# Optimization experiments

Measured on AMD Instinct MI355X. Metric: run time of the kernel, lower is better.

## Reference

```python
import jax, jax.numpy as jnp
import numpy as np

B, M, F, E = 64, 1024, 4, 256      # batch, memory length, tokens-per-memory-cell, emb_size
NW, HOPS, PL = 32000, 3, 128       # vocab, hops, profile_len


def _embed(table, idx):
    # nn.Embedding with padding_idx=0 -> index 0 maps to zero vector
    return table[idx] * (idx != 0)[..., None].astype(table.dtype)


def _gru_step(x, h, Wih, Whh, bih, bhh):
    # single-step PyTorch GRU cell
    gi = x @ Wih.T + bih
    gh = h @ Whh.T + bhh
    ir, iz, i_n = jnp.split(gi, 3, axis=-1)
    hr, hz, h_n = jnp.split(gh, 3, axis=-1)
    r = jax.nn.sigmoid(ir + hr)
    z = jax.nn.sigmoid(iz + hz)
    n = jnp.tanh(i_n + r * h_n)
    return (1.0 - z) * n + z * h


def setup_inputs() -> dict:
    key = jax.random.key(0)
    ks = jax.random.split(key, 13)
    # HOPS+1 unique embedding tables: A[0..hops-1] plus C[hops-1]; C[h]=tables[h+1] (weight tying)
    tables = (jax.random.normal(ks[0], (HOPS + 1, NW, E)) * 0.1).at[:, 0, :].set(0.0)
    s = 1.0 / np.sqrt(E)
    Wih = jax.random.uniform(ks[1], (3 * E, E), minval=-s, maxval=s)
    Whh = jax.random.uniform(ks[2], (3 * E, E), minval=-s, maxval=s)
    bih = jax.random.uniform(ks[3], (3 * E,), minval=-s, maxval=s)
    bhh = jax.random.uniform(ks[4], (3 * E,), minval=-s, maxval=s)
    sp = 1.0 / np.sqrt(PL)
    Wp = jax.random.uniform(ks[5], (E, PL), minval=-sp, maxval=sp)
    bp = jax.random.uniform(ks[6], (E,), minval=-sp, maxval=sp)
    sv = 1.0 / np.sqrt(2 * E)
    Wv = jax.random.uniform(ks[7], (NW, 2 * E), minval=-sv, maxval=sv)
    bv = jax.random.uniform(ks[8], (NW,), minval=-sv, maxval=sv)
    context = jax.random.randint(ks[9], (B, M, F), 0, NW)
    y_ = jax.random.randint(ks[10], (B,), 0, NW)
    h_ = jax.random.normal(ks[11], (1, B, E))
    profile_encoding = jax.random.normal(ks[12], (B, PL))
    return dict(tables=tables, Wih=Wih, Whh=Whh, bih=bih, bhh=bhh, Wp=Wp, bp=bp,
                Wv=Wv, bv=bv, context=context, y_=y_, h_=h_,
                profile_encoding=profile_encoding)


def reference(tables, Wih, Whh, bih, bhh, Wp, bp, Wv, bv, context, y_, h_, profile_encoding):
    # load_memory (eval mode: no word dropout): memories[h] = sum over F of table[h] embeddings
    ctx = context.reshape(B, M * F)
    mems = [_embed(tables[hop], ctx).reshape(B, M, F, E).sum(axis=2) for hop in range(HOPS + 1)]
    # decoder step
    m = _embed(tables[1], y_)                    # C[0](y_)
    h = _gru_step(m, h_[0], Wih, Whh, bih, bhh)  # [B, E]
    q = h
    p = p_vocab = p_resto = None
    for hop in range(HOPS):
        p_ = mems[hop] * q[:, None, :]           # [B, M, E] elementwise attention scores
        p = p_.sum(axis=2)                        # [B, M]
        attn = jax.nn.softmax(p, axis=1)
        o = jnp.einsum('bm,bme->be', attn, mems[hop + 1])
        if hop == 0:
            p_vocab = jnp.concatenate([h, o], axis=1) @ Wv.T + bv  # uses q[0]=h
        if hop == 1:
            enc = profile_encoding @ Wp.T + bp   # [B, E]
            p_resto = jnp.einsum('bme,be->bm', p_, enc)
        q = q + o
    return p, p_vocab, p_resto, h[None]          # p_ptr, p_vocab, p_resto, h [1,B,E]
```

## Files before the change

kernel.cpp:

```cpp
#include <hip/hip_runtime.h>
#include <cstdint>

#define B_ 64
#define M_ 1024
#define F_ 4
#define E_ 256
#define NW_ 32000
#define PL_ 128

#define P_OFF   0
#define PV_OFF  65536
#define PR_OFF  2113536
#define H_OFF   2179072

typedef unsigned short u16;
typedef unsigned int u32;

typedef __bf16 bf16x8 __attribute__((ext_vector_type(8)));
typedef float f32x4 __attribute__((ext_vector_type(4)));

__device__ __forceinline__ u16 f2bf(float f) {
    u32 x = __builtin_bit_cast(u32, f);
    u32 r = (x + 0x7fffu + ((x >> 16) & 1u)) >> 16;
    return (u16)r;
}

__device__ __forceinline__ bf16x8 pack_bf8(float4 a, float4 b) {
    union { u16 s[8]; bf16x8 v; } u;
    u.s[0] = f2bf(a.x); u.s[1] = f2bf(a.y); u.s[2] = f2bf(a.z); u.s[3] = f2bf(a.w);
    u.s[4] = f2bf(b.x); u.s[5] = f2bf(b.y); u.s[6] = f2bf(b.z); u.s[7] = f2bf(b.w);
    return u.v;
}

__global__ __launch_bounds__(256) void k_gru(
    const float* __restrict__ tables, const float* __restrict__ Wih,
    const float* __restrict__ Whh, const float* __restrict__ bih,
    const float* __restrict__ bhh, const float* __restrict__ Wp,
    const float* __restrict__ bp, const int* __restrict__ y,
    const float* __restrict__ h_, const float* __restrict__ pe,
    float* __restrict__ q0, float* __restrict__ enc, float* __restrict__ outh)
{
    int b = blockIdx.x, t = threadIdx.x;
    __shared__ float m_s[E_], h_s[E_], pe_s[PL_];
    int yb = y[b];
    m_s[t] = tables[(size_t)NW_ * E_ + (size_t)yb * E_ + t];
    h_s[t] = h_[b * E_ + t];
    if (t < PL_) pe_s[t] = pe[b * PL_ + t];
    __syncthreads();

    float g_i[3], g_h[3];
#pragma unroll
    for (int g = 0; g < 3; g++) {
        int j = g * E_ + t;
        float ai = bih[j];
        float ah = bhh[j];
        const float4* wi = (const float4*)(Wih + (size_t)j * E_);
        const float4* wh = (const float4*)(Whh + (size_t)j * E_);
#pragma unroll 8
        for (int e = 0; e < E_ / 4; e++) {
            float4 a = wi[e], c = wh[e];
            ai += a.x * m_s[4 * e] + a.y * m_s[4 * e + 1] +
                  a.z * m_s[4 * e + 2] + a.w * m_s[4 * e + 3];
            ah += c.x * h_s[4 * e] + c.y * h_s[4 * e + 1] +
                  c.z * h_s[4 * e + 2] + c.w * h_s[4 * e + 3];
        }
        g_i[g] = ai; g_h[g] = ah;
    }
    float r = 1.f / (1.f + expf(-(g_i[0] + g_h[0])));
    float z = 1.f / (1.f + expf(-(g_i[1] + g_h[1])));
    float n = tanhf(g_i[2] + r * g_h[2]);
    float hv = (1.f - z) * n + z * h_s[t];
    q0[b * E_ + t] = hv;
    outh[b * E_ + t] = hv;

    float ea = bp[t];
    const float4* wp = (const float4*)(Wp + (size_t)t * PL_);
#pragma unroll 8
    for (int p = 0; p < PL_ / 4; p++) {
        float4 a = wp[p];
        ea += a.x * pe_s[4 * p] + a.y * pe_s[4 * p + 1] +
              a.z * pe_s[4 * p + 2] + a.w * pe_s[4 * p + 3];
    }
    enc[b * E_ + t] = ea;
}

template <int MODE>
__global__ __launch_bounds__(256) void k_scores(
    const float* __restrict__ tab, const int* __restrict__ ctx,
    const float* __restrict__ q, const float* __restrict__ enc,
    float* __restrict__ p_ws, float* __restrict__ out)
{
    int b = blockIdx.y, grp = blockIdx.x;
    int lane = threadIdx.x & 63, w = threadIdx.x >> 6;
    int e0 = lane * 4;
    const float4 qv = *(const float4*)(q + b * E_ + e0);
    float4 qe = make_float4(0.f, 0.f, 0.f, 0.f);
    if (MODE == 1) {
        const float4 ev = *(const float4*)(enc + b * E_ + e0);
        qe = make_float4(qv.x * ev.x, qv.y * ev.y, qv.z * ev.z, qv.w * ev.w);
    }
    int mbase = grp * 32 + w * 8;
    const int4* cp = (const int4*)(ctx + ((size_t)b * M_ + mbase) * 4);
    int4 c[8];
#pragma unroll
    for (int i = 0; i < 8; i++) c[i] = cp[i];

    float pa[8], pr[8];
#pragma unroll
    for (int i = 0; i < 8; i++) {
        const float4 t0 = *(const float4*)(tab + (size_t)c[i].x * E_ + e0);
        const float4 t1 = *(const float4*)(tab + (size_t)c[i].y * E_ + e0);
        const float4 t2 = *(const float4*)(tab + (size_t)c[i].z * E_ + e0);
        const float4 t3 = *(const float4*)(tab + (size_t)c[i].w * E_ + e0);
        float rx = t0.x + t1.x + t2.x + t3.x;
        float ry = t0.y + t1.y + t2.y + t3.y;
        float rz = t0.z + t1.z + t2.z + t3.z;
        float rw = t0.w + t1.w + t2.w + t3.w;
        pa[i] = rx * qv.x + ry * qv.y + rz * qv.z + rw * qv.w;
        if (MODE == 1) pr[i] = rx * qe.x + ry * qe.y + rz * qe.z + rw * qe.w;
    }
#pragma unroll
    for (int o = 32; o > 0; o >>= 1) {
#pragma unroll
        for (int i = 0; i < 8; i++) {
            pa[i] += __shfl_xor(pa[i], o, 64);
            if (MODE == 1) pr[i] += __shfl_xor(pr[i], o, 64);
        }
    }
    if (lane == 0) {
#pragma unroll
        for (int i = 0; i < 8; i++) {
            if (MODE == 2) out[P_OFF + (size_t)b * M_ + mbase + i] = pa[i];
            else           p_ws[(size_t)b * M_ + mbase + i] = pa[i];
            if (MODE == 1) out[PR_OFF + (size_t)b * M_ + mbase + i] = pr[i];
        }
    }
}

__global__ __launch_bounds__(256) void k_soft(
    float* __restrict__ p_ws, const float* __restrict__ qcur,
    float* __restrict__ qnext)
{
    int b = blockIdx.x, t = threadIdx.x;
    __shared__ float red[256];
    float4 v = *(const float4*)(p_ws + (size_t)b * M_ + t * 4);
    float lm = fmaxf(fmaxf(v.x, v.y), fmaxf(v.z, v.w));
    red[t] = lm;
    __syncthreads();
    for (int s = 128; s > 0; s >>= 1) {
        if (t < s) red[t] = fmaxf(red[t], red[t + s]);
        __syncthreads();
    }
    float mx = red[0];
    __syncthreads();
    float e0 = expf(v.x - mx), e1 = expf(v.y - mx);
    float e2 = expf(v.z - mx), e3 = expf(v.w - mx);
    red[t] = e0 + e1 + e2 + e3;
    __syncthreads();
    for (int s = 128; s > 0; s >>= 1) {
        if (t < s) red[t] += red[t + s];
        __syncthreads();
    }
    float inv = 1.f / red[0];
    float4 o = make_float4(e0 * inv, e1 * inv, e2 * inv, e3 * inv);
    *(float4*)(p_ws + (size_t)b * M_ + t * 4) = o;
    qnext[b * E_ + t] = qcur[b * E_ + t];
}

__global__ __launch_bounds__(256) void k_opart(
    const float* __restrict__ tabC, const int* __restrict__ ctx,
    const float* __restrict__ attn, float* __restrict__ qnext)
{
    int b = blockIdx.y, ch = blockIdx.x;
    int lane = threadIdx.x & 63, w = threadIdx.x >> 6;
    int e0 = lane * 4;
    int mbase = ch * 32 + w * 8;

    const int4* cp = (const int4*)(ctx + ((size_t)b * M_ + mbase) * 4);
    int4 c[8];
#pragma unroll
    for (int i = 0; i < 8; i++) c[i] = cp[i];
    const float4* ap = (const float4*)(attn + (size_t)b * M_ + mbase);
    float4 a01 = ap[0], a23 = ap[1];
    float wg[8] = {a01.x, a01.y, a01.z, a01.w, a23.x, a23.y, a23.z, a23.w};

    float4 acc0 = make_float4(0.f, 0.f, 0.f, 0.f);
    float4 acc1 = make_float4(0.f, 0.f, 0.f, 0.f);
#pragma unroll
    for (int i = 0; i < 8; i += 2) {
        const float4 t0 = *(const float4*)(tabC + (size_t)c[i].x * E_ + e0);
        const float4 t1 = *(const float4*)(tabC + (size_t)c[i].y * E_ + e0);
        const float4 t2 = *(const float4*)(tabC + (size_t)c[i].z * E_ + e0);
        const float4 t3 = *(const float4*)(tabC + (size_t)c[i].w * E_ + e0);
        const float4 u0 = *(const float4*)(tabC + (size_t)c[i + 1].x * E_ + e0);
        const float4 u1 = *(const float4*)(tabC + (size_t)c[i + 1].y * E_ + e0);
        const float4 u2 = *(const float4*)(tabC + (size_t)c[i + 1].z * E_ + e0);
        const float4 u3 = *(const float4*)(tabC + (size_t)c[i + 1].w * E_ + e0);
        float w0 = wg[i], w1 = wg[i + 1];
        acc0.x += w0 * (t0.x + t1.x + t2.x + t3.x);
        acc0.y += w0 * (t0.y + t1.y + t2.y + t3.y);
        acc0.z += w0 * (t0.z + t1.z + t2.z + t3.z);
        acc0.w += w0 * (t0.w + t1.w + t2.w + t3.w);
        acc1.x += w1 * (u0.x + u1.x + u2.x + u3.x);
        acc1.y += w1 * (u0.y + u1.y + u2.y + u3.y);
        acc1.z += w1 * (u0.z + u1.z + u2.z + u3.z);
        acc1.w += w1 * (u0.w + u1.w + u2.w + u3.w);
    }
    float4 acc = make_float4(acc0.x + acc1.x, acc0.y + acc1.y,
                             acc0.z + acc1.z, acc0.w + acc1.w);
    __shared__ float red[4][E_];
    *(float4*)&red[w][e0] = acc;
    __syncthreads();
    int t = threadIdx.x;
    float s = red[0][t] + red[1][t] + red[2][t] + red[3][t];
    atomicAdd(qnext + b * E_ + t, s);
}

__global__ __launch_bounds__(256) void k_pvocab(
    const float* __restrict__ Wv, const float* __restrict__ bv,
    const float* __restrict__ q0, const float* __restrict__ q1,
    float* __restrict__ out)
{
    __shared__ u16 X[64 * 512];
    int t = threadIdx.x;
#pragma unroll
    for (int it = 0; it < 16; it++) {
        int id = t + it * 256;
        int bb = id >> 6, c = id & 63;
        float v[8];
        if (c < 32) {
            const float* s = q0 + bb * E_ + c * 8;
#pragma unroll
            for (int j = 0; j < 8; j++) v[j] = s[j];
        } else {
            const float* s1 = q1 + bb * E_ + (c - 32) * 8;
            const float* s0 = q0 + bb * E_ + (c - 32) * 8;
#pragma unroll
            for (int j = 0; j < 8; j++) v[j] = s1[j] - s0[j];
        }
        u32 ww[4];
#pragma unroll
        for (int j = 0; j < 4; j++)
            ww[j] = (u32)f2bf(v[2 * j]) | ((u32)f2bf(v[2 * j + 1]) << 16);
        uint4 uv = make_uint4(ww[0], ww[1], ww[2], ww[3]);
        *(uint4*)(&X[bb * 512 + ((c ^ (bb & 7)) << 3)]) = uv;
    }
    __syncthreads();

    int lane = t & 63, w = t >> 6;
    int n0 = blockIdx.x * 128 + w * 32;
    int l15 = lane & 15, quad = lane >> 4;
    f32x4 acc[4][2];
#pragma unroll
    for (int mt = 0; mt < 4; mt++)
#pragma unroll
        for (int nt = 0; nt < 2; nt++)
            acc[mt][nt] = f32x4{0.f, 0.f, 0.f, 0.f};

    for (int ks = 0; ks < 16; ks++) {
        bf16x8 a[4], bfr[2];
#pragma unroll
        for (int mt = 0; mt < 4; mt++) {
            int m = mt * 16 + l15;
            int c = ks * 4 + quad;
            a[mt] = *(const bf16x8*)(&X[m * 512 + ((c ^ (m & 7)) << 3)]);
        }
#pragma unroll
        for (int nt = 0; nt < 2; nt++) {
            int n = n0 + nt * 16 + l15;
            const float4* wp = (const float4*)(Wv + (size_t)n * 512 + ks * 32 + quad * 8);
            bfr[nt] = pack_bf8(wp[0], wp[1]);
        }
#pragma unroll
        for (int mt = 0; mt < 4; mt++)
#pragma unroll
            for (int nt = 0; nt < 2; nt++)
                acc[mt][nt] = __builtin_amdgcn_mfma_f32_16x16x32_bf16(
                    a[mt], bfr[nt], acc[mt][nt], 0, 0, 0);
    }
#pragma unroll
    for (int nt = 0; nt < 2; nt++) {
        int n = n0 + nt * 16 + l15;
        float bvv = bv[n];
#pragma unroll
        for (int mt = 0; mt < 4; mt++) {
#pragma unroll
            for (int j = 0; j < 4; j++) {
                int m = mt * 16 + quad * 4 + j;
                out[PV_OFF + (size_t)m * 32000 + n] = acc[mt][nt][j] + bvv;
            }
        }
    }
}

extern "C" void kernel_launch(void* const* d_in, const int* in_sizes, int n_in,
                              void* d_out, int out_size, void* d_ws, size_t ws_size,
                              hipStream_t stream)
{
    const float* tables = (const float*)d_in[0];
    const float* Wih = (const float*)d_in[1];
    const float* Whh = (const float*)d_in[2];
    const float* bih = (const float*)d_in[3];
    const float* bhh = (const float*)d_in[4];
    const float* Wp  = (const float*)d_in[5];
    const float* bp  = (const float*)d_in[6];
    const float* Wv  = (const float*)d_in[7];
    const float* bv  = (const float*)d_in[8];
    const int* ctx = (const int*)d_in[9];
    const int* y   = (const int*)d_in[10];
    const float* h_  = (const float*)d_in[11];
    const float* pe  = (const float*)d_in[12];
    float* out = (float*)d_out;

    float* Wf   = (float*)d_ws;
    float* q    = Wf;
    float* enc  = Wf + 65536;
    float* p_ws = Wf + 81920;

    const size_t TSZ = (size_t)NW_ * E_;

    k_gru<<<64, 256, 0, stream>>>(tables, Wih, Whh, bih, bhh, Wp, bp, y, h_, pe,
                                  q, enc, out + H_OFF);
    k_scores<0><<<dim3(32, 64), 256, 0, stream>>>(tables, ctx, q, enc, p_ws, out);
    k_soft<<<64, 256, 0, stream>>>(p_ws, q, q + 16384);
    k_opart<<<dim3(32, 64), 256, 0, stream>>>(tables + TSZ, ctx, p_ws, q + 16384);
    k_scores<1><<<dim3(32, 64), 256, 0, stream>>>(tables + TSZ, ctx, q + 16384,
                                                  enc, p_ws, out);
    k_soft<<<64, 256, 0, stream>>>(p_ws, q + 16384, q + 32768);
    k_opart<<<dim3(32, 64), 256, 0, stream>>>(tables + 2 * TSZ, ctx, p_ws, q + 32768);
    k_scores<2><<<dim3(32, 64), 256, 0, stream>>>(tables + 2 * TSZ, ctx, q + 32768,
                                                  enc, p_ws, out);
    k_pvocab<<<250, 256, 0, stream>>>(Wv, bv, q, q + 16384, out);
}
```

Measured before the change: 458.4 us.

## Convert embedding tables to bf16 and materialize mems1/mems2 once for reuse

Adds a per-call conversion kernel that casts the three used embedding tables to bf16, interleaving tables 1 and 2 per row. A new kernel gathers tables 1 and 2 together, writes the summed memory cells to bf16 buffers mems1/mems2, and computes the hop-0 output. Later hops read these materialized memories with contiguous loads instead of re-gathering four embedding rows per cell. This is meant to cut gather traffic, but it costs a full-table conversion pass every call and gives up precision to bf16 for the memories and the table-0 scores.

```diff
diff --git a/kernel.cpp b/kernel.cpp
--- a/kernel.cpp
+++ b/kernel.cpp
@@ -24,12 +24,51 @@
     u32 r = (x + 0x7fffu + ((x >> 16) & 1u)) >> 16;
     return (u16)r;
 }
-
+__device__ __forceinline__ float bflo(u32 v) {
+    return __builtin_bit_cast(float, v << 16);
+}
+__device__ __forceinline__ float bfhi(u32 v) {
+    return __builtin_bit_cast(float, v & 0xffff0000u);
+}
+__device__ __forceinline__ float dot8(uint4 u, float4 qa, float4 qb) {
+    return bflo(u.x) * qa.x + bfhi(u.x) * qa.y + bflo(u.y) * qa.z + bfhi(u.y) * qa.w +
+           bflo(u.z) * qb.x + bfhi(u.z) * qb.y + bflo(u.w) * qb.z + bfhi(u.w) * qb.w;
+}
+__device__ __forceinline__ void acc8(uint4 u, float* a) {
+    a[0] += bflo(u.x); a[1] += bfhi(u.x); a[2] += bflo(u.y); a[3] += bfhi(u.y);
+    a[4] += bflo(u.z); a[5] += bfhi(u.z); a[6] += bflo(u.w); a[7] += bfhi(u.w);
+}
+__device__ __forceinline__ uint4 pack8(const float* s) {
+    uint4 u;
+    u.x = (u32)f2bf(s[0]) | ((u32)f2bf(s[1]) << 16);
+    u.y = (u32)f2bf(s[2]) | ((u32)f2bf(s[3]) << 16);
+    u.z = (u32)f2bf(s[4]) | ((u32)f2bf(s[5]) << 16);
+    u.w = (u32)f2bf(s[6]) | ((u32)f2bf(s[7]) << 16);
+    return u;
+}
 __device__ __forceinline__ bf16x8 pack_bf8(float4 a, float4 b) {
     union { u16 s[8]; bf16x8 v; } u;
     u.s[0] = f2bf(a.x); u.s[1] = f2bf(a.y); u.s[2] = f2bf(a.z); u.s[3] = f2bf(a.w);
     u.s[4] = f2bf(b.x); u.s[5] = f2bf(b.y); u.s[6] = f2bf(b.z); u.s[7] = f2bf(b.w);
     return u.v;
+}
+
+__global__ __launch_bounds__(256) void k_conv(
+    const float* __restrict__ tables, u16* __restrict__ t0b, u16* __restrict__ t12)
+{
+    int t = blockIdx.y;
+    int c = blockIdx.x * 256 + threadIdx.x;
+    const float* src = tables + (size_t)t * NW_ * E_ + (size_t)c * 8;
+    float4 a = *(const float4*)src;
+    float4 b = *(const float4*)(src + 4);
+    float s[8] = {a.x, a.y, a.z, a.w, b.x, b.y, b.z, b.w};
+    uint4 u = pack8(s);
+    if (t == 0) {
+        *(uint4*)(t0b + (size_t)c * 8) = u;
+    } else {
+        int row = c >> 5, e = (c & 31) * 8;
+        *(uint4*)(t12 + (size_t)row * 512 + (t - 1) * 256 + e) = u;
+    }
 }
 
 __global__ __launch_bounds__(256) void k_gru(
@@ -52,8 +91,7 @@
 #pragma unroll
     for (int g = 0; g < 3; g++) {
         int j = g * E_ + t;
-        float ai = bih[j];
-        float ah = bhh[j];
+        float ai = bih[j], ah = bhh[j];
         const float4* wi = (const float4*)(Wih + (size_t)j * E_);
         const float4* wh = (const float4*)(Whh + (size_t)j * E_);
 #pragma unroll 8
@@ -84,57 +122,37 @@
     enc[b * E_ + t] = ea;
 }
 
-template <int MODE>
-__global__ __launch_bounds__(256) void k_scores(
-    const float* __restrict__ tab, const int* __restrict__ ctx,
-    const float* __restrict__ q, const float* __restrict__ enc,
-    float* __restrict__ p_ws, float* __restrict__ out)
+__global__ __launch_bounds__(256) void k_scores0(
+    const u16* __restrict__ t0b, const int* __restrict__ ctx,
+    const float* __restrict__ q, float* __restrict__ p_ws)
 {
     int b = blockIdx.y, grp = blockIdx.x;
     int lane = threadIdx.x & 63, w = threadIdx.x >> 6;
-    int e0 = lane * 4;
-    const float4 qv = *(const float4*)(q + b * E_ + e0);
-    float4 qe = make_float4(0.f, 0.f, 0.f, 0.f);
-    if (MODE == 1) {
-        const float4 ev = *(const float4*)(enc + b * E_ + e0);
-        qe = make_float4(qv.x * ev.x, qv.y * ev.y, qv.z * ev.z, qv.w * ev.w);
-    }
+    int h = lane >> 5, l32 = lane & 31, e0 = l32 * 8;
+    float4 qa = *(const float4*)(q + b * E_ + e0);
+    float4 qb = *(const float4*)(q + b * E_ + e0 + 4);
     int mbase = grp * 32 + w * 8;
     const int4* cp = (const int4*)(ctx + ((size_t)b * M_ + mbase) * 4);
     int4 c[8];
 #pragma unroll
     for (int i = 0; i < 8; i++) c[i] = cp[i];
 
-    float pa[8], pr[8];
+    float pa[8];
 #pragma unroll
     for (int i = 0; i < 8; i++) {
-        const float4 t0 = *(const float4*)(tab + (size_t)c[i].x * E_ + e0);
-        const float4 t1 = *(const float4*)(tab + (size_t)c[i].y * E_ + e0);
-        const float4 t2 = *(const float4*)(tab + (size_t)c[i].z * E_ + e0);
-        const float4 t3 = *(const float4*)(tab + (size_t)c[i].w * E_ + e0);
-        float rx = t0.x + t1.x + t2.x + t3.x;
-        float ry = t0.y + t1.y + t2.y + t3.y;
-        float rz = t0.z + t1.z + t2.z + t3.z;
-        float rw = t0.w + t1.w + t2.w + t3.w;
-        pa[i] = rx * qv.x + ry * qv.y + rz * qv.z + rw * qv.w;
-        if (MODE == 1) pr[i] = rx * qe.x + ry * qe.y + rz * qe.z + rw * qe.w;
-    }
-#pragma unroll
-    for (int o = 32; o > 0; o >>= 1) {
-#pragma unroll
-        for (int i = 0; i < 8; i++) {
-            pa[i] += __shfl_xor(pa[i], o, 64);
-            if (MODE == 1) pr[i] += __shfl_xor(pr[i], o, 64);
-        }
-    }
-    if (lane == 0) {
-#pragma unroll
-        for (int i = 0; i < 8; i++) {
-            if (MODE == 2) out[P_OFF + (size_t)b * M_ + mbase + i] = pa[i];
-            else           p_ws[(size_t)b * M_ + mbase + i] = pa[i];
-            if (MODE == 1) out[PR_OFF + (size_t)b * M_ + mbase + i] = pr[i];
-        }
-    }
+        int ia = h ? c[i].y : c[i].x;
+        int ib = h ? c[i].w : c[i].z;
+        uint4 ra = *(const uint4*)(t0b + (size_t)ia * E_ + e0);
+        uint4 rb = *(const uint4*)(t0b + (size_t)ib * E_ + e0);
+        pa[i] = dot8(ra, qa, qb) + dot8(rb, qa, qb);
+    }
+#pragma unroll
+    for (int o = 32; o > 0; o >>= 1)
+#pragma unroll
+        for (int i = 0; i < 8; i++) pa[i] += __shfl_xor(pa[i], o, 64);
+    if (lane == 0)
+#pragma unroll
+        for (int i = 0; i < 8; i++) p_ws[(size_t)b * M_ + mbase + i] = pa[i];
 }
 
 __global__ __launch_bounds__(256) void k_soft(
@@ -167,52 +185,123 @@
     qnext[b * E_ + t] = qcur[b * E_ + t];
 }
 
-__global__ __launch_bounds__(256) void k_opart(
-    const float* __restrict__ tabC, const int* __restrict__ ctx,
-    const float* __restrict__ attn, float* __restrict__ qnext)
+__global__ __launch_bounds__(256) void k_mems12(
+    const u16* __restrict__ t12, const int* __restrict__ ctx,
+    const float* __restrict__ attn0, u16* __restrict__ mems1,
+    u16* __restrict__ mems2, float* __restrict__ q1)
+{
+    int b = blockIdx.y, grp = blockIdx.x;
+    int lane = threadIdx.x & 63, w = threadIdx.x >> 6;
+    int h = lane >> 5, l32 = lane & 31, e0 = l32 * 8;
+    int mbase = grp * 32 + w * 8;
+    const int4* cp = (const int4*)(ctx + ((size_t)b * M_ + mbase) * 4);
+    int4 c[8];
+#pragma unroll
+    for (int i = 0; i < 8; i++) c[i] = cp[i];
+    float4 a01 = *(const float4*)(attn0 + (size_t)b * M_ + mbase);
+    float4 a23 = *(const float4*)(attn0 + (size_t)b * M_ + mbase + 4);
+    float wg[8] = {a01.x, a01.y, a01.z, a01.w, a23.x, a23.y, a23.z, a23.w};
+
+    u16* mout = h ? mems2 : mems1;
+    float o_acc[8] = {0, 0, 0, 0, 0, 0, 0, 0};
+#pragma unroll
+    for (int i = 0; i < 8; i++) {
+        size_t off = (size_t)h * 256 + e0;
+        uint4 r0 = *(const uint4*)(t12 + (size_t)c[i].x * 512 + off);
+        uint4 r1 = *(const uint4*)(t12 + (size_t)c[i].y * 512 + off);
+        uint4 r2 = *(const uint4*)(t12 + (size_t)c[i].z * 512 + off);
+        uint4 r3 = *(const uint4*)(t12 + (size_t)c[i].w * 512 + off);
+        float acc[8] = {0, 0, 0, 0, 0, 0, 0, 0};
+        acc8(r0, acc); acc8(r1, acc); acc8(r2, acc); acc8(r3, acc);
+        *(uint4*)(mout + ((size_t)(b * M_ + mbase + i)) * 256 + e0) = pack8(acc);
+        if (h == 0) {
+            float wgt = wg[i];
+#pragma unroll
+            for (int j = 0; j < 8; j++) o_acc[j] += wgt * acc[j];
+        }
+    }
+    __shared__ float red[4][E_];
+    if (h == 0)
+#pragma unroll
+        for (int j = 0; j < 8; j++) red[w][e0 + j] = o_acc[j];
+    __syncthreads();
+    int t = threadIdx.x;
+    float s = red[0][t] + red[1][t] + red[2][t] + red[3][t];
+    atomicAdd(q1 + b * E_ + t, s);
+}
+
+template <int MODE>
+__global__ __launch_bounds__(256) void k_sscores(
+    const u16* __restrict__ mems, const float* __restrict__ q,
+    const float* __restrict__ enc, float* __restrict__ p_ws,
+    float* __restrict__ out)
+{
+    int b = blockIdx.y, grp = blockIdx.x;
+    int lane = threadIdx.x & 63, w = threadIdx.x >> 6;
+    int h = lane >> 5, l32 = lane & 31, e0 = l32 * 8;
+    float4 qa = *(const float4*)(q + b * E_ + e0);
+    float4 qb = *(const float4*)(q + b * E_ + e0 + 4);
+    float4 ea4 = make_float4(0, 0, 0, 0), eb4 = make_float4(0, 0, 0, 0);
+    if (MODE == 1) {
+        float4 ev = *(const float4*)(enc + b * E_ + e0);
+        float4 ew = *(const float4*)(enc + b * E_ + e0 + 4);
+        ea4 = make_float4(qa.x * ev.x, qa.y * ev.y, qa.z * ev.z, qa.w * ev.w);
+        eb4 = make_float4(qb.x * ew.x, qb.y * ew.y, qb.z * ew.z, qb.w * ew.w);
+    }
+    int mbase = grp * 32 + w * 8;
+    float pa[4], pr[4];
+#pragma unroll
+    for (int i = 0; i < 4; i++) {
+        int m = mbase + 2 * i + h;
+        uint4 r = *(const uint4*)(mems + ((size_t)(b * M_ + m)) * 256 + e0);
+        pa[i] = dot8(r, qa, qb);
+        if (MODE == 1) pr[i] = dot8(r, ea4, eb4);
+    }
+#pragma unroll
+    for (int o = 16; o > 0; o >>= 1)
+#pragma unroll
+        for (int i = 0; i < 4; i++) {
+            pa[i] += __shfl_xor(pa[i], o, 64);
+            if (MODE == 1) pr[i] += __shfl_xor(pr[i], o, 64);
+        }
+    if (l32 == 0) {
+#pragma unroll
+        for (int i = 0; i < 4; i++) {
+            int m = mbase + 2 * i + h;
+            if (MODE == 2) out[P_OFF + (size_t)b * M_ + m] = pa[i];
+            else           p_ws[(size_t)b * M_ + m] = pa[i];
+            if (MODE == 1) out[PR_OFF + (size_t)b * M_ + m] = pr[i];
+        }
+    }
+}
+
+__global__ __launch_bounds__(256) void k_so(
+    const u16* __restrict__ mems, const float* __restrict__ attn,
+    float* __restrict__ qnext)
 {
     int b = blockIdx.y, ch = blockIdx.x;
     int lane = threadIdx.x & 63, w = threadIdx.x >> 6;
-    int e0 = lane * 4;
-    int mbase = ch * 32 + w * 8;
-
-    const int4* cp = (const int4*)(ctx + ((size_t)b * M_ + mbase) * 4);
-    int4 c[8];
-#pragma unroll
-    for (int i = 0; i < 8; i++) c[i] = cp[i];
-    const float4* ap = (const float4*)(attn + (size_t)b * M_ + mbase);
-    float4 a01 = ap[0], a23 = ap[1];
-    float wg[8] = {a01.x, a01.y, a01.z, a01.w, a23.x, a23.y, a23.z, a23.w};
-
-    float4 acc0 = make_float4(0.f, 0.f, 0.f, 0.f);
-    float4 acc1 = make_float4(0.f, 0.f, 0.f, 0.f);
-#pragma unroll
-    for (int i = 0; i < 8; i += 2) {
-        const float4 t0 = *(const float4*)(tabC + (size_t)c[i].x * E_ + e0);
-        const float4 t1 = *(const float4*)(tabC + (size_t)c[i].y * E_ + e0);
-        const float4 t2 = *(const float4*)(tabC + (size_t)c[i].z * E_ + e0);
-        const float4 t3 = *(const float4*)(tabC + (size_t)c[i].w * E_ + e0);
-        const float4 u0 = *(const float4*)(tabC + (size_t)c[i + 1].x * E_ + e0);
-        const float4 u1 = *(const float4*)(tabC + (size_t)c[i + 1].y * E_ + e0);
-        const float4 u2 = *(const float4*)(tabC + (size_t)c[i + 1].z * E_ + e0);
-        const float4 u3 = *(const float4*)(tabC + (size_t)c[i + 1].w * E_ + e0);
-        float w0 = wg[i], w1 = wg[i + 1];
-        acc0.x += w0 * (t0.x + t1.x + t2.x + t3.x);
-        acc0.y += w0 * (t0.y + t1.y + t2.y + t3.y);
-        acc0.z += w0 * (t0.z + t1.z + t2.z + t3.z);
-        acc0.w += w0 * (t0.w + t1.w + t2.w + t3.w);
-        acc1.x += w1 * (u0.x + u1.x + u2.x + u3.x);
-        acc1.y += w1 * (u0.y + u1.y + u2.y + u3.y);
-        acc1.z += w1 * (u0.z + u1.z + u2.z + u3.z);
-        acc1.w += w1 * (u0.w + u1.w + u2.w + u3.w);
-    }
-    float4 acc = make_float4(acc0.x + acc1.x, acc0.y + acc1.y,
-                             acc0.z + acc1.z, acc0.w + acc1.w);
-    __shared__ float red[4][E_];
-    *(float4*)&red[w][e0] = acc;
+    int h = lane >> 5, l32 = lane & 31, e0 = l32 * 8;
+    int m0 = ch * 128;
+    float acc[8] = {0, 0, 0, 0, 0, 0, 0, 0};
+    for (int i = 0; i < 16; i++) {
+        int m = m0 + i * 8 + w * 2 + h;
+        float wgt = attn[(size_t)b * M_ + m];
+        uint4 r = *(const uint4*)(mems + ((size_t)(b * M_ + m)) * 256 + e0);
+        acc[0] += wgt * bflo(r.x); acc[1] += wgt * bfhi(r.x);
+        acc[2] += wgt * bflo(r.y); acc[3] += wgt * bfhi(r.y);
+        acc[4] += wgt * bflo(r.z); acc[5] += wgt * bfhi(r.z);
+        acc[6] += wgt * bflo(r.w); acc[7] += wgt * bfhi(r.w);
+    }
+    __shared__ float red[8][E_];
+    int hw = threadIdx.x >> 5;
+#pragma unroll
+    for (int j = 0; j < 8; j++) red[hw][e0 + j] = acc[j];
     __syncthreads();
     int t = threadIdx.x;
-    float s = red[0][t] + red[1][t] + red[2][t] + red[3][t];
+    float s = 0.f;
+#pragma unroll
+    for (int k = 0; k < 8; k++) s += red[k][t];
     atomicAdd(qnext + b * E_ + t, s);
 }
 
@@ -238,11 +327,7 @@
 #pragma unroll
             for (int j = 0; j < 8; j++) v[j] = s1[j] - s0[j];
         }
-        u32 ww[4];
-#pragma unroll
-        for (int j = 0; j < 4; j++)
-            ww[j] = (u32)f2bf(v[2 * j]) | ((u32)f2bf(v[2 * j + 1]) << 16);
-        uint4 uv = make_uint4(ww[0], ww[1], ww[2], ww[3]);
+        uint4 uv = pack8(v);
         *(uint4*)(&X[bb * 512 + ((c ^ (bb & 7)) << 3)]) = uv;
     }
     __syncthreads();
@@ -316,19 +401,22 @@
     float* q    = Wf;
     float* enc  = Wf + 65536;
     float* p_ws = Wf + 81920;
-
-    const size_t TSZ = (size_t)NW_ * E_;
-
+    char* base  = (char*)d_ws + 589824;
+    u16* t0b    = (u16*)base;
+    u16* t12    = (u16*)(base + 16384000);
+    u16* mems1  = (u16*)(base + 16384000 + 32768000);
+    u16* mems2  = (u16*)(base + 16384000 + 32768000 + 33554432);
+
+    k_conv<<<dim3(4000, 3), 256, 0, stream>>>(tables, t0b, t12);
     k_gru<<<64, 256, 0, stream>>>(tables, Wih, Whh, bih, bhh, Wp, bp, y, h_, pe,
                                   q, enc, out + H_OFF);
-    k_scores<0><<<dim3(32, 64), 256, 0, stream>>>(tables, ctx, q, enc, p_ws, out);
+    k_scores0<<<dim3(32, 64), 256, 0, stream>>>(t0b, ctx, q, p_ws);
     k_soft<<<64, 256, 0, stream>>>(p_ws, q, q + 16384);
-    k_opart<<<dim3(32, 64), 256, 0, stream>>>(tables + TSZ, ctx, p_ws, q + 16384);
-    k_scores<1><<<dim3(32, 64), 256, 0, stream>>>(tables + TSZ, ctx, q + 16384,
-                                                  enc, p_ws, out);
+    k_mems12<<<dim3(32, 64), 256, 0, stream>>>(t12, ctx, p_ws, mems1, mems2,
+                                               q + 16384);
+    k_sscores<1><<<dim3(32, 64), 256, 0, stream>>>(mems1, q + 16384, enc, p_ws, out);
     k_soft<<<64, 256, 0, stream>>>(p_ws, q + 16384, q + 32768);
-    k_opart<<<dim3(32, 64), 256, 0, stream>>>(tables + 2 * TSZ, ctx, p_ws, q + 32768);
-    k_scores<2><<<dim3(32, 64), 256, 0, stream>>>(tables + 2 * TSZ, ctx, q + 32768,
-                                                  enc, p_ws, out);
+    k_so<<<dim3(8, 64), 256, 0, stream>>>(mems2, p_ws, q + 32768);
+    k_sscores<2><<<dim3(32, 64), 256, 0, stream>>>(mems2, q + 32768, enc, p_ws, out);
     k_pvocab<<<250, 256, 0, stream>>>(Wv, bv, q, q + 16384, out);
 }
```

New measurement: 399.3 us. 12.9% less time.
